# Performance work log

Measured on AMD Instinct MI355X. Metric: run time of the kernel, lower is better.

The kernel has to match this reference:

```python
import jax, jax.numpy as jnp
import numpy as np

E_QUBITS = 8  # embedding dim == number of qubits


def _iqp_amplitudes(x):
    """Statevector amplitudes of qml.IQPEmbedding(x) applied to |0..0>.

    x: [..., E] real. Returns [..., 2^E] complex64.
    Circuit: H on all wires, RZ(x_i) on wire i, MultiRZ(x_i*x_j) on all pairs i<j.
    For basis state z with signs s_i = (-1)^{z_i}:
      amp(z) = 2^{-E/2} * exp(i * phi(z)),
      phi(z) = -1/2 * sum_i x_i s_i - 1/2 * sum_{i<j} x_i x_j s_i s_j
             = -L/2 - (L^2 - ||x||^2)/4,  with L = sum_i x_i s_i.
    """
    E = x.shape[-1]
    z = jnp.arange(2 ** E)
    bits = (z[:, None] >> jnp.arange(E)[None, :]) & 1          # [2^E, E]
    s = (1.0 - 2.0 * bits).astype(x.dtype)                      # (-1)^{z_i}
    L = x @ s.T                                                 # [..., 2^E]
    sq = jnp.sum(x * x, axis=-1, keepdims=True)                 # ||x||^2
    phase = -0.5 * L - 0.25 * (L * L - sq)
    return jnp.exp(1j * phase) * (2.0 ** (-E / 2.0))            # complex64


def setup_inputs() -> dict:
    key = jax.random.key(0)
    kq, kk, kv = jax.random.split(key, 3)
    B, S, E = 16, 1024, E_QUBITS
    return {
        "Q": jax.random.normal(kq, (B, S, E), dtype=jnp.float32),
        "K": jax.random.normal(kk, (B, S, E), dtype=jnp.float32),
        "V": jax.random.normal(kv, (B, S, E), dtype=jnp.float32),
    }


def reference(Q, K, V):
    # Pure-state amplitudes for every token (IQP embedding). [B,S,2^E] complex
    aq = _iqp_amplitudes(Q)
    ak = _iqp_amplitudes(K)
    # Fidelity of pure states: |<psi_q|psi_k>|^2, batched Gram matrix.
    ip = jnp.einsum("bid,bjd->bij", jnp.conj(aq), ak)          # [B,S,S] complex
    fid = jnp.real(ip * jnp.conj(ip))                           # [B,S,S] float32
    attn = 2.0 * fid - 1.0
    return jnp.einsum("bij,bje->bie", attn, V)                  # [B,S,E]
```

## Files before the change

### kernel.cpp

```cpp
#include <hip/hip_runtime.h>
#include <hip/hip_bf16.h>
#include <stdint.h>

#define NB 16
#define S_LEN 1024
#define E_Q 8

typedef float v4f __attribute__((ext_vector_type(4)));
typedef short v8s __attribute__((ext_vector_type(8)));
typedef int   v4i __attribute__((ext_vector_type(4)));

__global__ __launch_bounds__(256) void build_tables(
    const float* __restrict__ Q, const float* __restrict__ K,
    int8_t* __restrict__ Aq, int8_t* __restrict__ Kt)
{
    const int which = blockIdx.y;
    const float* X = which ? K : Q;

    const int tok = blockIdx.x * 16 + (threadIdx.x >> 4);
    const int hi  = threadIdx.x & 15;
    const int zb  = hi * 16;

    const float* x = X + tok * E_Q;
    float xv[E_Q]; float sq = 0.f;
#pragma unroll
    for (int i = 0; i < E_Q; ++i) { xv[i] = x[i]; sq += xv[i] * xv[i]; }
    const float qsq = 0.25f * sq;

    float L = xv[0] + xv[1] + xv[2] + xv[3];
#pragma unroll
    for (int i = 4; i < 8; ++i) L += ((hi >> (i - 4)) & 1) ? -xv[i] : xv[i];

    __align__(16) int8_t cb[16];
    __align__(16) int8_t sb[16];

    {
        const float phi = fmaf(-0.25f, L * L, fmaf(-0.5f, L, qsq));
        float s, c; __sincosf(phi, &s, &c);
        cb[0] = (int8_t)__float2int_rn(127.f * c);
        sb[0] = (int8_t)__float2int_rn(127.f * s);
    }
#pragma unroll
    for (int n = 1; n < 16; ++n) {
        const int g  = n ^ (n >> 1);
        const int gp = (n - 1) ^ ((n - 1) >> 1);
        const int t  = __builtin_ctz(g ^ gp);
        const float twox = 2.0f * xv[t];
        L = ((g >> t) & 1) ? (L - twox) : (L + twox);
        const float phi = fmaf(-0.25f, L * L, fmaf(-0.5f, L, qsq));
        float s, c; __sincosf(phi, &s, &c);
        cb[g] = (int8_t)__float2int_rn(127.f * c);
        sb[g] = (int8_t)__float2int_rn(127.f * s);
    }

    if (which == 0) {
        int8_t* dst = Aq + (size_t)tok * 512;
        *(uint4*)(dst + zb)       = *(const uint4*)cb;
        *(uint4*)(dst + 256 + zb) = *(const uint4*)sb;
    } else {
        __align__(16) int8_t nb[16];
#pragma unroll
        for (int i = 0; i < 16; ++i) nb[i] = (int8_t)(-cb[i]);
        int8_t* dst = Kt + (size_t)tok * 768;
        *(uint4*)(dst + zb)       = *(const uint4*)cb;
        *(uint4*)(dst + 256 + zb) = *(const uint4*)sb;
        *(uint4*)(dst + 512 + zb) = *(const uint4*)nb;
    }
}

__global__ __launch_bounds__(256, 2) void qk_pv(
    const int8_t* __restrict__ Aq, const int8_t* __restrict__ Kt,
    const float* __restrict__ V, float* __restrict__ part)
{
    __shared__ __align__(16) char smem[49152];
    uint16_t* lattn = (uint16_t*)smem;
    uint16_t* lVt   = (uint16_t*)(smem + 34816);

    const int jblk = blockIdx.x, iblk = blockIdx.y, b = blockIdx.z;
    const int tid  = threadIdx.x;
    const int lane = tid & 63, wv = tid >> 6;
    const int wKj = wv >> 1, wQi = wv & 1;
    const int r15 = lane & 15, qq = lane >> 4;

    const int ssw   = ((tid & 3) ^ ((tid >> 2) & 3)) << 4;
    const int baseA = (tid >> 2) * 512 + ssw;
    const int baseK = (tid >> 2) * 768 + ssw;
    const int ldst  = tid * 16;

    const int swz16 = (qq ^ (r15 & 3)) << 4;
    const int offA  = wQi * 4096 + r15 * 64 + swz16;
    const int offK  = 8192 + wKj * 4096 + r15 * 64 + swz16;

    const int8_t* gA = Aq + (size_t)(b * S_LEN + iblk * 128) * 512;
    const int8_t* gK = Kt + (size_t)(b * S_LEN + jblk * 128) * 768;

    v4i accRe[4][4], accIm[4][4];
#pragma unroll
    for (int nj = 0; nj < 4; ++nj)
#pragma unroll
        for (int mi = 0; mi < 4; ++mi) {
            accRe[nj][mi] = (v4i)0;
            accIm[nj][mi] = (v4i)0;
        }

#define STAGE(cc, bb)                                                          \
    {                                                                          \
        const int lb0 = (bb) * 24576 + ldst;                                   \
        _Pragma("unroll")                                                      \
        for (int p = 0; p < 2; ++p) {                                          \
            __builtin_amdgcn_global_load_lds(                                  \
                (const __attribute__((address_space(1))) void*)(gA + (cc) * 64 + baseA + p * 32768), \
                (__attribute__((address_space(3))) void*)(smem + lb0 + p * 4096), 16, 0, 0); \
            __builtin_amdgcn_global_load_lds(                                  \
                (const __attribute__((address_space(1))) void*)(gK + (cc) * 64 + baseK + p * 49152), \
                (__attribute__((address_space(3))) void*)(smem + lb0 + 8192 + p * 4096), 16, 0, 0); \
            __builtin_amdgcn_global_load_lds(                                  \
                (const __attribute__((address_space(1))) void*)(gK + 256 + (cc) * 64 + baseK + p * 49152), \
                (__attribute__((address_space(3))) void*)(smem + lb0 + 16384 + p * 4096), 16, 0, 0); \
        }                                                                      \
    }

    STAGE(0, 0)
    STAGE(1, 1)

#pragma unroll
    for (int c = 0; c < 8; ++c) {
        if (c == 7) { asm volatile("s_waitcnt vmcnt(0)" ::: "memory"); }
        else        { asm volatile("s_waitcnt vmcnt(6)" ::: "memory"); }
        __builtin_amdgcn_s_barrier();
        asm volatile("" ::: "memory");

        {
            const int8_t* lb = (const int8_t*)smem + ((c & 1) ? 24576 : 0);
            v4i qF[4];
#pragma unroll
            for (int mi = 0; mi < 4; ++mi)
                qF[mi] = *(const v4i*)(lb + offA + mi * 1024);
            __builtin_amdgcn_s_setprio(1);
#pragma unroll
            for (int nj = 0; nj < 4; ++nj) {
                const v4i k0 = *(const v4i*)(lb + offK + nj * 1024);
                const v4i k1 = *(const v4i*)(lb + offK + 8192 + nj * 1024);
#pragma unroll
                for (int mi = 0; mi < 4; ++mi) {
                    accRe[nj][mi] = __builtin_amdgcn_mfma_i32_16x16x64_i8(k0, qF[mi], accRe[nj][mi], 0, 0, 0);
                    accIm[nj][mi] = __builtin_amdgcn_mfma_i32_16x16x64_i8(k1, qF[mi], accIm[nj][mi], 0, 0, 0);
                }
            }
            __builtin_amdgcn_s_setprio(0);
        }

        asm volatile("" ::: "memory");
        __builtin_amdgcn_s_barrier();
        if (c < 6) STAGE(c + 2, c & 1)
    }
#undef STAGE

    __syncthreads();

    const float4 vreg = ((const float4*)(V + ((size_t)b * S_LEN + jblk * 128) * E_Q))[tid];

    const float sc2 = 3.0517578125e-05f / 260144641.0f;
#pragma unroll
    for (int nj = 0; nj < 4; ++nj) {
#pragma unroll
        for (int mi = 0; mi < 4; ++mi) {
            uint64_t pk = 0;
#pragma unroll
            for (int rg = 0; rg < 4; ++rg) {
                const float rf  = (float)accRe[nj][mi][rg];
                const float imf = (float)accIm[nj][mi][rg];
                const float a   = fmaf(rf * rf + imf * imf, sc2, -1.0f);
                __hip_bfloat16 ab = __float2bfloat16(a);
                pk |= (uint64_t)(*(const uint16_t*)&ab) << (16 * rg);
            }
            const int i  = wQi * 64 + mi * 16 + r15;
            const int j0 = wKj * 64 + nj * 16 + qq * 4;
            *(uint64_t*)&lattn[i * 136 + j0] = pk;
        }
    }
    {
        const int j = tid >> 1, eh = (tid & 1) * 4;
        const float vv[4] = {vreg.x, vreg.y, vreg.z, vreg.w};
#pragma unroll
        for (int c2 = 0; c2 < 4; ++c2) {
            __hip_bfloat16 vb = __float2bfloat16(vv[c2]);
            lVt[(eh + c2) * 136 + j] = *(const uint16_t*)&vb;
        }
    }
    __syncthreads();

    v8s bfr[4];
#pragma unroll
    for (int ks3 = 0; ks3 < 4; ++ks3)
        bfr[ks3] = *(const v8s*)&lVt[r15 * 136 + ks3 * 32 + qq * 8];

    float* pout = part + ((size_t)jblk << 17)
                + (((size_t)b << 10) + iblk * 128) * E_Q;
#pragma unroll
    for (int mt = 0; mt < 2; ++mt) {
        const int rowbase = (wv * 2 + mt) * 16;
        v4f accO = (v4f)0.f;
#pragma unroll
        for (int ks3 = 0; ks3 < 4; ++ks3) {
            const v8s af = *(const v8s*)&lattn[(rowbase + r15) * 136 + ks3 * 32 + qq * 8];
            accO = __builtin_amdgcn_mfma_f32_16x16x32_bf16(af, bfr[ks3], accO, 0, 0, 0);
        }
        if (r15 < E_Q) {
            const int i0 = rowbase + qq * 4;
#pragma unroll
            for (int rg = 0; rg < 4; ++rg)
                pout[(i0 + rg) * E_Q + r15] = accO[rg];
        }
    }
}

__global__ __launch_bounds__(256) void reduce_out(
    const float4* __restrict__ part, float4* __restrict__ out)
{
    const int idx = blockIdx.x * 256 + threadIdx.x;
    float4 s = part[idx];
#pragma unroll
    for (int k = 1; k < 8; ++k) {
        const float4 p = part[k * 32768 + idx];
        s.x += p.x; s.y += p.y; s.z += p.z; s.w += p.w;
    }
    out[idx] = s;
}

extern "C" void kernel_launch(void* const* d_in, const int* in_sizes, int n_in,
                              void* d_out, int out_size, void* d_ws, size_t ws_size,
                              hipStream_t stream) {
    const float* Q = (const float*)d_in[0];
    const float* K = (const float*)d_in[1];
    const float* V = (const float*)d_in[2];

    int8_t* Aq   = (int8_t*)d_ws;
    int8_t* Kt   = (int8_t*)((char*)d_ws + (size_t)8 * 1024 * 1024);
    float*  part = (float*)((char*)d_ws + (size_t)20 * 1024 * 1024);

    build_tables<<<dim3(NB * S_LEN / 16, 2), 256, 0, stream>>>(Q, K, Aq, Kt);
    qk_pv<<<dim3(S_LEN / 128, S_LEN / 128, NB), 256, 0, stream>>>(Aq, Kt, V, part);
    reduce_out<<<dim3(128), 256, 0, stream>>>((const float4*)part, (float4*)d_out);
}
```

Measured before the change: 92.04 us.

## Compute complex Gram via four real sub-products, drop negated cosine table

The K table no longer stores a negated cosine block, so both Q and K use a compact [cos|sin] layout. The imaginary part is formed as the difference of two separate int8 MFMA accumulators (cos·sin minus sin·cos), and the real part accumulates cos·cos plus sin·sin. This cuts K-table global writes and loads by a third and halves the pipeline iteration count. In exchange it needs an extra accumulator set (more VGPR/AGPR pressure) and a larger LDS buffer.

```diff
diff --git a/kernel.cpp b/kernel.cpp
--- a/kernel.cpp
+++ b/kernel.cpp
@@ -53,26 +53,16 @@
         sb[g] = (int8_t)__float2int_rn(127.f * s);
     }
 
-    if (which == 0) {
-        int8_t* dst = Aq + (size_t)tok * 512;
-        *(uint4*)(dst + zb)       = *(const uint4*)cb;
-        *(uint4*)(dst + 256 + zb) = *(const uint4*)sb;
-    } else {
-        __align__(16) int8_t nb[16];
-#pragma unroll
-        for (int i = 0; i < 16; ++i) nb[i] = (int8_t)(-cb[i]);
-        int8_t* dst = Kt + (size_t)tok * 768;
-        *(uint4*)(dst + zb)       = *(const uint4*)cb;
-        *(uint4*)(dst + 256 + zb) = *(const uint4*)sb;
-        *(uint4*)(dst + 512 + zb) = *(const uint4*)nb;
-    }
+    int8_t* dst = (which ? Kt : Aq) + (size_t)tok * 512;
+    *(uint4*)(dst + zb)       = *(const uint4*)cb;
+    *(uint4*)(dst + 256 + zb) = *(const uint4*)sb;
 }
 
 __global__ __launch_bounds__(256, 2) void qk_pv(
     const int8_t* __restrict__ Aq, const int8_t* __restrict__ Kt,
     const float* __restrict__ V, float* __restrict__ part)
 {
-    __shared__ __align__(16) char smem[49152];
+    __shared__ __align__(16) char smem[65536];
     uint16_t* lattn = (uint16_t*)smem;
     uint16_t* lVt   = (uint16_t*)(smem + 34816);
 
@@ -83,40 +73,43 @@
     const int r15 = lane & 15, qq = lane >> 4;
 
     const int ssw   = ((tid & 3) ^ ((tid >> 2) & 3)) << 4;
-    const int baseA = (tid >> 2) * 512 + ssw;
-    const int baseK = (tid >> 2) * 768 + ssw;
+    const int gbase = (tid >> 2) * 512 + ssw;
     const int ldst  = tid * 16;
 
     const int swz16 = (qq ^ (r15 & 3)) << 4;
-    const int offA  = wQi * 4096 + r15 * 64 + swz16;
-    const int offK  = 8192 + wKj * 4096 + r15 * 64 + swz16;
+    const int offQ  = (wQi * 64 + r15) * 64 + swz16;
+    const int offK  = 16384 + (wKj * 64 + r15) * 64 + swz16;
 
     const int8_t* gA = Aq + (size_t)(b * S_LEN + iblk * 128) * 512;
-    const int8_t* gK = Kt + (size_t)(b * S_LEN + jblk * 128) * 768;
-
-    v4i accRe[4][4], accIm[4][4];
+    const int8_t* gK = Kt + (size_t)(b * S_LEN + jblk * 128) * 512;
+
+    v4i accRe[4][4], accP3[4][4], accP4[4][4];
 #pragma unroll
     for (int nj = 0; nj < 4; ++nj)
 #pragma unroll
         for (int mi = 0; mi < 4; ++mi) {
             accRe[nj][mi] = (v4i)0;
-            accIm[nj][mi] = (v4i)0;
+            accP3[nj][mi] = (v4i)0;
+            accP4[nj][mi] = (v4i)0;
         }
 
 #define STAGE(cc, bb)                                                          \
     {                                                                          \
-        const int lb0 = (bb) * 24576 + ldst;                                   \
+        const int lb0 = (bb) * 32768 + ldst;                                   \
         _Pragma("unroll")                                                      \
         for (int p = 0; p < 2; ++p) {                                          \
             __builtin_amdgcn_global_load_lds(                                  \
-                (const __attribute__((address_space(1))) void*)(gA + (cc) * 64 + baseA + p * 32768), \
+                (const __attribute__((address_space(1))) void*)(gA + (cc) * 64 + gbase + p * 32768), \
                 (__attribute__((address_space(3))) void*)(smem + lb0 + p * 4096), 16, 0, 0); \
             __builtin_amdgcn_global_load_lds(                                  \
-                (const __attribute__((address_space(1))) void*)(gK + (cc) * 64 + baseK + p * 49152), \
+                (const __attribute__((address_space(1))) void*)(gA + 256 + (cc) * 64 + gbase + p * 32768), \
                 (__attribute__((address_space(3))) void*)(smem + lb0 + 8192 + p * 4096), 16, 0, 0); \
             __builtin_amdgcn_global_load_lds(                                  \
-                (const __attribute__((address_space(1))) void*)(gK + 256 + (cc) * 64 + baseK + p * 49152), \
+                (const __attribute__((address_space(1))) void*)(gK + (cc) * 64 + gbase + p * 32768), \
                 (__attribute__((address_space(3))) void*)(smem + lb0 + 16384 + p * 4096), 16, 0, 0); \
+            __builtin_amdgcn_global_load_lds(                                  \
+                (const __attribute__((address_space(1))) void*)(gK + 256 + (cc) * 64 + gbase + p * 32768), \
+                (__attribute__((address_space(3))) void*)(smem + lb0 + 24576 + p * 4096), 16, 0, 0); \
         }                                                                      \
     }
 
@@ -124,27 +117,34 @@
     STAGE(1, 1)
 
 #pragma unroll
-    for (int c = 0; c < 8; ++c) {
-        if (c == 7) { asm volatile("s_waitcnt vmcnt(0)" ::: "memory"); }
-        else        { asm volatile("s_waitcnt vmcnt(6)" ::: "memory"); }
+    for (int c = 0; c < 4; ++c) {
+        if (c == 3) { asm volatile("s_waitcnt vmcnt(0)" ::: "memory"); }
+        else        { asm volatile("s_waitcnt vmcnt(8)" ::: "memory"); }
         __builtin_amdgcn_s_barrier();
         asm volatile("" ::: "memory");
 
         {
-            const int8_t* lb = (const int8_t*)smem + ((c & 1) ? 24576 : 0);
-            v4i qF[4];
-#pragma unroll
-            for (int mi = 0; mi < 4; ++mi)
-                qF[mi] = *(const v4i*)(lb + offA + mi * 1024);
+            const int8_t* lb = (const int8_t*)smem + ((c & 1) ? 32768 : 0);
+            v4i qc[4], qs[4];
+#pragma unroll
+            for (int mi = 0; mi < 4; ++mi) {
+                qc[mi] = *(const v4i*)(lb + offQ + mi * 1024);
+                qs[mi] = *(const v4i*)(lb + 8192 + offQ + mi * 1024);
+            }
             __builtin_amdgcn_s_setprio(1);
 #pragma unroll
             for (int nj = 0; nj < 4; ++nj) {
-                const v4i k0 = *(const v4i*)(lb + offK + nj * 1024);
-                const v4i k1 = *(const v4i*)(lb + offK + 8192 + nj * 1024);
+                const v4i kc = *(const v4i*)(lb + offK + nj * 1024);
+                const v4i ks = *(const v4i*)(lb + offK + 8192 + nj * 1024);
 #pragma unroll
                 for (int mi = 0; mi < 4; ++mi) {
-                    accRe[nj][mi] = __builtin_amdgcn_mfma_i32_16x16x64_i8(k0, qF[mi], accRe[nj][mi], 0, 0, 0);
-                    accIm[nj][mi] = __builtin_amdgcn_mfma_i32_16x16x64_i8(k1, qF[mi], accIm[nj][mi], 0, 0, 0);
+                    accRe[nj][mi] = __builtin_amdgcn_mfma_i32_16x16x64_i8(kc, qc[mi], accRe[nj][mi], 0, 0, 0);
+                    accP4[nj][mi] = __builtin_amdgcn_mfma_i32_16x16x64_i8(kc, qs[mi], accP4[nj][mi], 0, 0, 0);
+                }
+#pragma unroll
+                for (int mi = 0; mi < 4; ++mi) {
+                    accRe[nj][mi] = __builtin_amdgcn_mfma_i32_16x16x64_i8(ks, qs[mi], accRe[nj][mi], 0, 0, 0);
+                    accP3[nj][mi] = __builtin_amdgcn_mfma_i32_16x16x64_i8(ks, qc[mi], accP3[nj][mi], 0, 0, 0);
                 }
             }
             __builtin_amdgcn_s_setprio(0);
@@ -152,7 +152,7 @@
 
         asm volatile("" ::: "memory");
         __builtin_amdgcn_s_barrier();
-        if (c < 6) STAGE(c + 2, c & 1)
+        if (c < 2) STAGE(c + 2, c & 1)
     }
 #undef STAGE
 
@@ -169,7 +169,7 @@
 #pragma unroll
             for (int rg = 0; rg < 4; ++rg) {
                 const float rf  = (float)accRe[nj][mi][rg];
-                const float imf = (float)accIm[nj][mi][rg];
+                const float imf = (float)(accP3[nj][mi][rg] - accP4[nj][mi][rg]);
                 const float a   = fmaf(rf * rf + imf * imf, sc2, -1.0f);
                 __hip_bfloat16 ab = __float2bfloat16(a);
                 pk |= (uint64_t)(*(const uint16_t*)&ab) << (16 * rg);
@@ -237,7 +237,7 @@
 
     int8_t* Aq   = (int8_t*)d_ws;
     int8_t* Kt   = (int8_t*)((char*)d_ws + (size_t)8 * 1024 * 1024);
-    float*  part = (float*)((char*)d_ws + (size_t)20 * 1024 * 1024);
+    float*  part = (float*)((char*)d_ws + (size_t)16 * 1024 * 1024);
 
     build_tables<<<dim3(NB * S_LEN / 16, 2), 256, 0, stream>>>(Q, K, Aq, Kt);
     qk_pv<<<dim3(S_LEN / 128, S_LEN / 128, NB), 256, 0, stream>>>(Aq, Kt, V, part);
```

New measurement: 92.17 us. About the same (+0.1%).

## Enlarge QK tile to 256 query rows with 512-thread blocks

Applied to the files above, without the earlier changes.

The fused QK/PV kernel now covers 256 query rows by 128 key rows per block with 8 waves instead of 128x128 with 4 waves. This halves how many times each K tile is loaded per batch and reduces the block count. Shared memory grows to about 72KB and the staging layout and waitcnt values change to match. The extra threads zero the padding rows of the transposed V tile. The larger LDS footprint and block size may reduce how many blocks fit on a CU and leave fewer blocks to spread across CUs.

```diff
diff --git a/kernel.cpp b/kernel.cpp
--- a/kernel.cpp
+++ b/kernel.cpp
@@ -68,18 +68,18 @@
     }
 }
 
-__global__ __launch_bounds__(256, 2) void qk_pv(
+__global__ __launch_bounds__(512, 2) void qk_pv(
     const int8_t* __restrict__ Aq, const int8_t* __restrict__ Kt,
     const float* __restrict__ V, float* __restrict__ part)
 {
-    __shared__ __align__(16) char smem[49152];
+    __shared__ __align__(16) char smem[73984];
     uint16_t* lattn = (uint16_t*)smem;
-    uint16_t* lVt   = (uint16_t*)(smem + 34816);
+    uint16_t* lVt   = (uint16_t*)(smem + 69632);
 
     const int jblk = blockIdx.x, iblk = blockIdx.y, b = blockIdx.z;
     const int tid  = threadIdx.x;
     const int lane = tid & 63, wv = tid >> 6;
-    const int wKj = wv >> 1, wQi = wv & 1;
+    const int wQi = wv >> 1, wKj = wv & 1;
     const int r15 = lane & 15, qq = lane >> 4;
 
     const int ssw   = ((tid & 3) ^ ((tid >> 2) & 3)) << 4;
@@ -88,10 +88,10 @@
     const int ldst  = tid * 16;
 
     const int swz16 = (qq ^ (r15 & 3)) << 4;
-    const int offA  = wQi * 4096 + r15 * 64 + swz16;
-    const int offK  = 8192 + wKj * 4096 + r15 * 64 + swz16;
-
-    const int8_t* gA = Aq + (size_t)(b * S_LEN + iblk * 128) * 512;
+    const int offA  = (wQi * 64 + r15) * 64 + swz16;
+    const int offK0 = 16384 + (wKj * 64 + r15) * 64 + swz16;
+
+    const int8_t* gA = Aq + (size_t)(b * S_LEN + iblk * 256) * 512;
     const int8_t* gK = Kt + (size_t)(b * S_LEN + jblk * 128) * 768;
 
     v4i accRe[4][4], accIm[4][4];
@@ -105,19 +105,19 @@
 
 #define STAGE(cc, bb)                                                          \
     {                                                                          \
-        const int lb0 = (bb) * 24576 + ldst;                                   \
-        _Pragma("unroll")                                                      \
-        for (int p = 0; p < 2; ++p) {                                          \
-            __builtin_amdgcn_global_load_lds(                                  \
-                (const __attribute__((address_space(1))) void*)(gA + (cc) * 64 + baseA + p * 32768), \
-                (__attribute__((address_space(3))) void*)(smem + lb0 + p * 4096), 16, 0, 0); \
-            __builtin_amdgcn_global_load_lds(                                  \
-                (const __attribute__((address_space(1))) void*)(gK + (cc) * 64 + baseK + p * 49152), \
-                (__attribute__((address_space(3))) void*)(smem + lb0 + 8192 + p * 4096), 16, 0, 0); \
-            __builtin_amdgcn_global_load_lds(                                  \
-                (const __attribute__((address_space(1))) void*)(gK + 256 + (cc) * 64 + baseK + p * 49152), \
-                (__attribute__((address_space(3))) void*)(smem + lb0 + 16384 + p * 4096), 16, 0, 0); \
-        }                                                                      \
+        const int lb0 = (bb) * 32768 + ldst;                                   \
+        __builtin_amdgcn_global_load_lds(                                      \
+            (const __attribute__((address_space(1))) void*)(gA + (cc) * 64 + baseA), \
+            (__attribute__((address_space(3))) void*)(smem + lb0), 16, 0, 0);  \
+        __builtin_amdgcn_global_load_lds(                                      \
+            (const __attribute__((address_space(1))) void*)(gA + (cc) * 64 + baseA + 65536), \
+            (__attribute__((address_space(3))) void*)(smem + lb0 + 8192), 16, 0, 0); \
+        __builtin_amdgcn_global_load_lds(                                      \
+            (const __attribute__((address_space(1))) void*)(gK + (cc) * 64 + baseK), \
+            (__attribute__((address_space(3))) void*)(smem + lb0 + 16384), 16, 0, 0); \
+        __builtin_amdgcn_global_load_lds(                                      \
+            (const __attribute__((address_space(1))) void*)(gK + 256 + (cc) * 64 + baseK), \
+            (__attribute__((address_space(3))) void*)(smem + lb0 + 24576), 16, 0, 0); \
     }
 
     STAGE(0, 0)
@@ -126,12 +126,12 @@
 #pragma unroll
     for (int c = 0; c < 8; ++c) {
         if (c == 7) { asm volatile("s_waitcnt vmcnt(0)" ::: "memory"); }
-        else        { asm volatile("s_waitcnt vmcnt(6)" ::: "memory"); }
+        else        { asm volatile("s_waitcnt vmcnt(4)" ::: "memory"); }
         __builtin_amdgcn_s_barrier();
         asm volatile("" ::: "memory");
 
         {
-            const int8_t* lb = (const int8_t*)smem + ((c & 1) ? 24576 : 0);
+            const int8_t* lb = (const int8_t*)smem + ((c & 1) ? 32768 : 0);
             v4i qF[4];
 #pragma unroll
             for (int mi = 0; mi < 4; ++mi)
@@ -139,8 +139,8 @@
             __builtin_amdgcn_s_setprio(1);
 #pragma unroll
             for (int nj = 0; nj < 4; ++nj) {
-                const v4i k0 = *(const v4i*)(lb + offK + nj * 1024);
-                const v4i k1 = *(const v4i*)(lb + offK + 8192 + nj * 1024);
+                const v4i k0 = *(const v4i*)(lb + offK0 + nj * 1024);
+                const v4i k1 = *(const v4i*)(lb + offK0 + 8192 + nj * 1024);
 #pragma unroll
                 for (int mi = 0; mi < 4; ++mi) {
                     accRe[nj][mi] = __builtin_amdgcn_mfma_i32_16x16x64_i8(k0, qF[mi], accRe[nj][mi], 0, 0, 0);
@@ -158,7 +158,9 @@
 
     __syncthreads();
 
-    const float4 vreg = ((const float4*)(V + ((size_t)b * S_LEN + jblk * 128) * E_Q))[tid];
+    float4 vreg;
+    if (tid < 256)
+        vreg = ((const float4*)(V + ((size_t)b * S_LEN + jblk * 128) * E_Q))[tid];
 
     const float sc2 = 3.0517578125e-05f / 260144641.0f;
 #pragma unroll
@@ -180,12 +182,19 @@
         }
     }
     {
-        const int j = tid >> 1, eh = (tid & 1) * 4;
-        const float vv[4] = {vreg.x, vreg.y, vreg.z, vreg.w};
-#pragma unroll
-        for (int c2 = 0; c2 < 4; ++c2) {
-            __hip_bfloat16 vb = __float2bfloat16(vv[c2]);
-            lVt[(eh + c2) * 136 + j] = *(const uint16_t*)&vb;
+        if (tid < 256) {
+            const int j = tid >> 1, eh = (tid & 1) * 4;
+            const float vv[4] = {vreg.x, vreg.y, vreg.z, vreg.w};
+#pragma unroll
+            for (int c2 = 0; c2 < 4; ++c2) {
+                __hip_bfloat16 vb = __float2bfloat16(vv[c2]);
+                lVt[(eh + c2) * 136 + j] = *(const uint16_t*)&vb;
+            }
+        } else {
+            const int j = (tid - 256) >> 1, eh = (tid & 1) * 4;
+#pragma unroll
+            for (int c2 = 0; c2 < 4; ++c2)
+                lVt[(8 + eh + c2) * 136 + j] = 0;
         }
     }
     __syncthreads();
@@ -196,7 +205,7 @@
         bfr[ks3] = *(const v8s*)&lVt[r15 * 136 + ks3 * 32 + qq * 8];
 
     float* pout = part + ((size_t)jblk << 17)
-                + (((size_t)b << 10) + iblk * 128) * E_Q;
+                + ((size_t)b << 13) + (iblk << 11);
 #pragma unroll
     for (int mt = 0; mt < 2; ++mt) {
         const int rowbase = (wv * 2 + mt) * 16;
@@ -240,6 +249,6 @@
     float*  part = (float*)((char*)d_ws + (size_t)20 * 1024 * 1024);
 
     build_tables<<<dim3(NB * S_LEN / 16, 2), 256, 0, stream>>>(Q, K, Aq, Kt);
-    qk_pv<<<dim3(S_LEN / 128, S_LEN / 128, NB), 256, 0, stream>>>(Aq, Kt, V, part);
+    qk_pv<<<dim3(S_LEN / 128, S_LEN / 256, NB), 512, 0, stream>>>(Aq, Kt, V, part);
     reduce_out<<<dim3(128), 256, 0, stream>>>((const float4*)part, (float4*)d_out);
 }
```

Measured after the change: 93.50 us. No clear change (+1.6%).
